# Kernel tuning notes

Hardware: AMD Instinct MI355X
Metric: run time of the kernel (lower is better)

The kernel has to match this reference:

```python
import jax, jax.numpy as jnp
import numpy as np
import itertools

G = 24  # octahedral rotation group order (reflection=False)
K = 3   # kernel_size

def _octahedral_tables():
    # 24 proper rotations of the cube as signed permutation matrices (det=+1)
    mats = []
    for perm in itertools.permutations(range(3)):
        for signs in itertoolsools_product if False else itertools.product((1, -1), repeat=3):
            M = np.zeros((3, 3), dtype=np.int64)
            for i, p in enumerate(perm):
                M[i, p] = signs[i]
            if round(np.linalg.det(M)) == 1:
                mats.append(M)
    mats = np.stack(mats)  # (24,3,3)
    key = {tuple(m.flatten()): i for i, m in enumerate(mats)}
    # Cayley-derived index shift: shift[g][h] = index of R_g^{-1} R_h
    shift = np.zeros((G, G), dtype=np.int64)
    for g in range(G):
        Rg_inv = mats[g].T  # orthogonal
        for h in range(G):
            shift[g, h] = key[tuple((Rg_inv @ mats[h]).flatten())]
    # spatial rotation gather indices: rotated K'(x) = K(R^{-1}(x-c)+c)
    c = (K - 1) // 2
    coords = np.stack(np.meshgrid(np.arange(K), np.arange(K), np.arange(K), indexing='ij'), -1).reshape(-1, 3)
    rot_idx = np.zeros((G, K ** 3), dtype=np.int64)
    for g in range(G):
        src = (coords - c) @ mats[g]  # equals R_g^{-1} @ (x-c) row-wise
        src = src + c
        rot_idx[g] = src[:, 0] * K * K + src[:, 1] * K + src[:, 2]
    return shift, rot_idx

SHIFT, ROT_IDX = _octahedral_tables()

def setup_inputs() -> dict:
    key = jax.random.key(0)
    k1, k2, k3, k4, k5 = jax.random.split(key, 5)
    B, I, O, H = 2, 16, 16, 32
    fan_g = I  # kaiming-ish scale for g_weight last dim
    fan_t = K ** 3
    return {
        'x': jax.random.normal(k1, (B, I, G, H, H, H), dtype=jnp.float32),
        'g_weight': jax.random.normal(k2, (G, O, I), dtype=jnp.float32) * (1.0 / np.sqrt(fan_g)),
        't_weight': jax.random.normal(k3, (O, 1, K, K, K), dtype=jnp.float32) * (1.0 / np.sqrt(fan_t)),
        'g_bias': jax.random.normal(k4, (1, O, 1, 1, 1, 1), dtype=jnp.float32) * 0.1,
        't_bias': jax.random.normal(k5, (1,), dtype=jnp.float32) * 0.1,
    }

def reference(x, g_weight, t_weight, g_bias, t_bias):
    O = g_weight.shape[1]
    B, _, _, H, W, D = x.shape
    # filter bank G: permute group axis of g_weight per group element -> (G_z, G_g, O, I)
    gfb = g_weight[SHIFT]
    # filter bank T: rotated depthwise kernels -> (O, G, K^3)
    tfb = t_weight.reshape(O, K ** 3)[:, ROT_IDX]
    w = tfb.reshape(O * G, 1, K, K, K)
    # group-equivariant channel mix + bias
    y = jnp.einsum('bighwd,zgoi->bozhwd', x, gfb) + g_bias
    y = y.reshape(B, O * G, H, W, D)
    # depthwise conv3d with groups = O*G, padding=1, stride=1
    out = jax.lax.conv_general_dilated(
        y, w, window_strides=(1, 1, 1), padding=[(1, 1)] * 3,
        dimension_numbers=('NCDHW', 'OIDHW', 'NCDHW'),
        feature_group_count=O * G) + t_bias[0]
    out = out.reshape(B, O, G, out.shape[2], out.shape[3], out.shape[4])
    return jax.nn.leaky_relu(out, negative_slope=0.01)
```

## Files before the change

### kernel.cpp

```cpp
#include <hip/hip_runtime.h>
#include <hip/hip_bf16.h>
#include <stdint.h>

typedef unsigned short ushortx;
typedef __attribute__((ext_vector_type(8))) short bs8;
typedef __attribute__((ext_vector_type(4))) float f32x4;

struct Tab {
    int shift[24][24];
    int rot[24][27];
};

constexpr Tab make_tab() {
    Tab t{};
    int mats[24][3][3] = {};
    {
        const int perms[6][3] = {{0,1,2},{0,2,1},{1,0,2},{1,2,0},{2,0,1},{2,1,0}};
        const int sgns[8][3]  = {{1,1,1},{1,1,-1},{1,-1,1},{1,-1,-1},
                                 {-1,1,1},{-1,1,-1},{-1,-1,1},{-1,-1,-1}};
        int n = 0;
        for (int pi = 0; pi < 6; ++pi)
            for (int si = 0; si < 8; ++si) {
                int M[3][3] = {};
                for (int i = 0; i < 3; ++i) M[i][perms[pi][i]] = sgns[si][i];
                int det = M[0][0]*(M[1][1]*M[2][2]-M[1][2]*M[2][1])
                        - M[0][1]*(M[1][0]*M[2][2]-M[1][2]*M[2][0])
                        + M[0][2]*(M[1][0]*M[2][1]-M[1][1]*M[2][0]);
                if (det == 1) {
                    for (int i = 0; i < 3; ++i)
                        for (int j = 0; j < 3; ++j) mats[n][i][j] = M[i][j];
                    ++n;
                }
            }
    }
    for (int g = 0; g < 24; ++g)
        for (int h = 0; h < 24; ++h) {
            int P[3][3] = {};
            for (int i = 0; i < 3; ++i)
                for (int j = 0; j < 3; ++j) {
                    int s = 0;
                    for (int e = 0; e < 3; ++e) s += mats[g][e][i] * mats[h][e][j];
                    P[i][j] = s;
                }
            for (int k = 0; k < 24; ++k) {
                bool eq = true;
                for (int i = 0; i < 3; ++i)
                    for (int j = 0; j < 3; ++j)
                        if (mats[k][i][j] != P[i][j]) eq = false;
                if (eq) t.shift[g][h] = k;
            }
        }
    for (int g = 0; g < 24; ++g)
        for (int j = 0; j < 27; ++j) {
            int co[3] = { j/9 - 1, (j/3)%3 - 1, j%3 - 1 };
            int src[3] = {};
            for (int d = 0; d < 3; ++d) {
                int s = 0;
                for (int e = 0; e < 3; ++e) s += co[e] * mats[g][e][d];
                src[d] = s + 1;
            }
            t.rot[g][j] = src[0]*9 + src[1]*3 + src[2];
        }
    return t;
}

__constant__ Tab TAB = make_tab();

#define GG 24
#define OO 16
#define II 16
#define PVOL 32768
#define MCH 384
#define KCH 384
#define KG  48

__device__ __forceinline__ unsigned f2bfu(float f) {
    union { float f; unsigned u; } a; a.f = f;
    unsigned r = a.u + 0x7FFFu + ((a.u >> 16) & 1u);
    return r >> 16;
}
__device__ __forceinline__ float bfu2f(unsigned h) {
    union { unsigned u; float f; } a; a.u = h << 16;
    return a.f;
}

#define GLOAD16(gp, lp) \
    __builtin_amdgcn_global_load_lds((const __attribute__((address_space(1))) void*)(gp), \
                                     (__attribute__((address_space(3))) void*)(lp), 16, 0, 0)

__global__ void build_weights2(const float* __restrict__ gw, const float* __restrict__ tw,
                               ushortx* __restrict__ w2, float* __restrict__ wt) {
    int idx = blockIdx.x * 256 + threadIdx.x;
    if (idx < MCH * KCH) {
        int m = idx / KCH, k = idx % KCH;
        int o = m / GG, z = m % GG;
        int i = k / GG, g = k % GG;
        float w = gw[TAB.shift[z][g] * (OO * II) + o * II + i];
        unsigned h = f2bfu(w);
        unsigned l = f2bfu(w - bfu2f(h));
        size_t base = (size_t)m * 768 + (k >> 5) * 64 + (k & 31);
        w2[base]      = (ushortx)h;
        w2[base + 32] = (ushortx)l;
    } else {
        int r = idx - MCH * KCH;
        if (r < MCH * 27) {
            int c = r / 27, j = r % 27;
            wt[r] = tw[(c / GG) * 27 + TAB.rot[c % GG][j]];
        }
    }
}

__global__ __launch_bounds__(256) void convert_x(const float* __restrict__ X,
                                                 uint4* __restrict__ Xhi,
                                                 uint4* __restrict__ Xlo) {
    const int n0 = blockIdx.x * 256, kg = blockIdx.y, b = blockIdx.z;
    __shared__ float s[8][260];
    const int t = threadIdx.x;
    const float* Xb = X + ((size_t)b * KCH + kg * 8) * PVOL;

    {
        const int r0 = t >> 6, c4 = (t & 63) * 4;
        float4 v0 = *(const float4*)&Xb[(size_t)r0 * PVOL + n0 + c4];
        float4 v1 = *(const float4*)&Xb[(size_t)(r0 + 4) * PVOL + n0 + c4];
        *(float4*)&s[r0][c4] = v0;
        *(float4*)&s[r0 + 4][c4] = v1;
    }
    __syncthreads();

    const int n = t;
    float f0 = s[0][n], f1 = s[1][n], f2 = s[2][n], f3 = s[3][n];
    float f4 = s[4][n], f5 = s[5][n], f6 = s[6][n], f7 = s[7][n];

    unsigned h0 = f2bfu(f0), h1 = f2bfu(f1), h2 = f2bfu(f2), h3 = f2bfu(f3);
    unsigned h4 = f2bfu(f4), h5 = f2bfu(f5), h6 = f2bfu(f6), h7 = f2bfu(f7);
    uint4 H = { h0 | (h1 << 16), h2 | (h3 << 16), h4 | (h5 << 16), h6 | (h7 << 16) };

    unsigned l0 = f2bfu(f0 - bfu2f(h0)), l1 = f2bfu(f1 - bfu2f(h1));
    unsigned l2 = f2bfu(f2 - bfu2f(h2)), l3 = f2bfu(f3 - bfu2f(h3));
    unsigned l4 = f2bfu(f4 - bfu2f(h4)), l5 = f2bfu(f5 - bfu2f(h5));
    unsigned l6 = f2bfu(f6 - bfu2f(h6)), l7 = f2bfu(f7 - bfu2f(h7));
    uint4 L = { l0 | (l1 << 16), l2 | (l3 << 16), l4 | (l5 << 16), l6 | (l7 << 16) };

    const size_t ci = ((size_t)(b * KG + kg)) * PVOL + n0 + n;
    Xhi[ci] = H;
    Xlo[ci] = L;
}

__global__ __launch_bounds__(256) void gemm_mfma(const ushortx* __restrict__ W2,
                                                 const uint4* __restrict__ Xhi,
                                                 const uint4* __restrict__ Xlo,
                                                 const float* __restrict__ gbias,
                                                 float* __restrict__ Y) {
    __shared__ ushortx As[2][8192];
    __shared__ ushortx Bs[2][8192];
    const int b = blockIdx.z, m0 = blockIdx.y * 128, n0 = blockIdx.x * 128;
    const int tid = threadIdx.x, lane = tid & 63, wave = tid >> 6;
    const int wr = wave >> 1, wc = wave & 1;
    const int l15 = lane & 15, lq = lane >> 4;

    f32x4 acc[4][4] = {};

    const char* Ab = (const char*)W2 + (size_t)m0 * 1536;
    const uint4* XH = Xhi + (size_t)b * KG * PVOL + n0;
    const uint4* XL = Xlo + (size_t)b * KG * PVOL + n0;

#define STAGE(bb, it)                                                          \
    {                                                                          \
        _Pragma("unroll")                                                      \
        for (int j = 0; j < 4; ++j) {                                          \
            int inst = j * 4 + wave;                                           \
            int fb = inst * 1024 + (lane << 4);                                \
            int row = fb >> 7;                                                 \
            int sch = ((fb >> 4) & 7) ^ (row & 7);                             \
            GLOAD16(Ab + (size_t)row * 1536 + (it) * 128 + sch * 16,           \
                    (char*)&As[bb][0] + fb);                                   \
            const uint4* plane = (sch < 4) ? XH : XL;                          \
            GLOAD16(plane + ((size_t)((it) * 4 + (sch & 3))) * PVOL + row,     \
                    (char*)&Bs[bb][0] + fb);                                   \
        }                                                                      \
    }

    STAGE(0, 0);

    int cur = 0;
    for (int it = 0; it < 12; ++it) {
        if (it < 11) {
            STAGE(cur ^ 1, it + 1);
            asm volatile("s_waitcnt vmcnt(8)" ::: "memory");
        } else {
            asm volatile("s_waitcnt vmcnt(0)" ::: "memory");
        }
        __builtin_amdgcn_sched_barrier(0);
        __builtin_amdgcn_s_barrier();
        __builtin_amdgcn_sched_barrier(0);

        bs8 ah[4], al[4], bh[4], bl[4];
        #pragma unroll
        for (int f = 0; f < 4; ++f) {
            int rowA = wr * 64 + f * 16 + l15;
            int swzA = (rowA & 7) << 4;
            ah[f] = *(const bs8*)((const char*)&As[cur][0] + rowA * 128 + ((lq * 16) ^ swzA));
            al[f] = *(const bs8*)((const char*)&As[cur][0] + rowA * 128 + ((64 + lq * 16) ^ swzA));
            int rowB = wc * 64 + f * 16 + l15;
            int swzB = (rowB & 7) << 4;
            bh[f] = *(const bs8*)((const char*)&Bs[cur][0] + rowB * 128 + ((lq * 16) ^ swzB));
            bl[f] = *(const bs8*)((const char*)&Bs[cur][0] + rowB * 128 + ((64 + lq * 16) ^ swzB));
        }
        #pragma unroll
        for (int fm = 0; fm < 4; ++fm)
            #pragma unroll
            for (int fn = 0; fn < 4; ++fn) {
                acc[fm][fn] = __builtin_amdgcn_mfma_f32_16x16x32_bf16(ah[fm], bh[fn], acc[fm][fn], 0, 0, 0);
                acc[fm][fn] = __builtin_amdgcn_mfma_f32_16x16x32_bf16(ah[fm], bl[fn], acc[fm][fn], 0, 0, 0);
                acc[fm][fn] = __builtin_amdgcn_mfma_f32_16x16x32_bf16(al[fm], bh[fn], acc[fm][fn], 0, 0, 0);
            }

        asm volatile("" ::: "memory");
        __builtin_amdgcn_s_barrier();
        asm volatile("" ::: "memory");
        cur ^= 1;
    }
#undef STAGE

    float* Yp = Y + (size_t)b * MCH * PVOL;
    #pragma unroll
    for (int fm = 0; fm < 4; ++fm)
        #pragma unroll
        for (int j = 0; j < 4; ++j) {
            int m = m0 + wr * 64 + fm * 16 + lq * 4 + j;
            float bias = gbias[m / GG];
            #pragma unroll
            for (int fn = 0; fn < 4; ++fn) {
                int n = n0 + wc * 64 + fn * 16 + l15;
                Yp[(size_t)m * PVOL + n] = acc[fm][fn][j] + bias;
            }
        }
}

__global__ __launch_bounds__(256) void dwconv(const float* __restrict__ Y,
                                              const float* __restrict__ Wt,
                                              const float* __restrict__ tb,
                                              float* __restrict__ O) {
    const int x0 = blockIdx.x * 4;
    const int c  = blockIdx.y;
    const int b  = blockIdx.z;
    const float* __restrict__ Yc = Y + ((size_t)(b * MCH + c)) * PVOL;
    float* __restrict__ Oc = O + ((size_t)(b * MCH + c)) * PVOL;

    __shared__ float s[6][34][40];
    __shared__ float taps[27];
    const int t = threadIdx.x;

    {
        float4 z4 = {0.f, 0.f, 0.f, 0.f};
        float4* sp = (float4*)s;
        for (int i = t; i < 2040; i += 256) sp[i] = z4;
    }
    if (t < 27) taps[t] = Wt[c * 27 + t];
    __syncthreads();

    const int y  = t >> 3;
    const int z0 = (t & 7) * 4;

    {
        float4 r[6];
        #pragma unroll
        for (int lx = 0; lx < 6; ++lx) {
            int x = x0 - 1 + lx;
            bool ok = (x >= 0 && x < 32);
            r[lx] = ok ? *(const float4*)&Yc[(size_t)x * 1024 + y * 32 + z0]
                       : (float4){0.f, 0.f, 0.f, 0.f};
        }
        #pragma unroll
        for (int lx = 0; lx < 6; ++lx)
            *(float4*)&s[lx][1 + y][4 + z0] = r[lx];
    }
    __syncthreads();

    const float t0 = tb[0];
    float w[27];
    #pragma unroll
    for (int j = 0; j < 27; ++j) w[j] = taps[j];

    float Wn[3][3][6];

    #define LOADWIN(slot, plane)                                              \
        {                                                                     \
            _Pragma("unroll")                                                 \
            for (int dy = 0; dy < 3; ++dy) {                                  \
                float4 a = *(const float4*)&s[plane][y + dy][z0];             \
                float4 bq = *(const float4*)&s[plane][y + dy][z0 + 4];        \
                float4 cq = *(const float4*)&s[plane][y + dy][z0 + 8];        \
                Wn[slot][dy][0] = a.w;                                        \
                Wn[slot][dy][1] = bq.x; Wn[slot][dy][2] = bq.y;               \
                Wn[slot][dy][3] = bq.z; Wn[slot][dy][4] = bq.w;               \
                Wn[slot][dy][5] = cq.x;                                       \
            }                                                                 \
        }

    LOADWIN(0, 0)
    LOADWIN(1, 1)

    #pragma unroll
    for (int xi = 0; xi < 4; ++xi) {
        LOADWIN((xi + 2) % 3, (xi + 2))
        const int s0 = xi % 3, s1 = (xi + 1) % 3, s2 = (xi + 2) % 3;
        float4 o;
        #pragma unroll
        for (int zz = 0; zz < 4; ++zz) {
            float a0 = 0.f, a1 = 0.f, a2 = 0.f;
            #pragma unroll
            for (int dy = 0; dy < 3; ++dy)
                #pragma unroll
                for (int dc = 0; dc < 3; ++dc) {
                    a0 += Wn[s0][dy][zz + dc] * w[dy * 3 + dc];
                    a1 += Wn[s1][dy][zz + dc] * w[9 + dy * 3 + dc];
                    a2 += Wn[s2][dy][zz + dc] * w[18 + dy * 3 + dc];
                }
            float v = a0 + a1 + a2 + t0;
            o[zz] = (v > 0.f) ? v : 0.01f * v;
        }
        *(float4*)&Oc[(size_t)(x0 + xi) * 1024 + y * 32 + z0] = o;
    }
    #undef LOADWIN
}

__global__ void build_weights(const float* __restrict__ gw, const float* __restrict__ tw,
                              float* __restrict__ wmix, float* __restrict__ wt) {
    int idx = blockIdx.x * 256 + threadIdx.x;
    if (idx < MCH * KCH) {
        int c = idx / KCH, k = idx % KCH;
        int o = c / GG, z = c % GG;
        int i = k / GG, g = k % GG;
        wmix[idx] = gw[TAB.shift[z][g] * (OO * II) + o * II + i];
    } else {
        int r = idx - MCH * KCH;
        if (r < MCH * 27) {
            int c = r / 27, j = r % 27;
            wt[r] = tw[(c / GG) * 27 + TAB.rot[c % GG][j]];
        }
    }
}

#define BM 128
#define BN 128
#define BK 16

__global__ __launch_bounds__(256) void gemm_mix(const float* __restrict__ A,
                                                const float* __restrict__ X,
                                                const float* __restrict__ gbias,
                                                float* __restrict__ Y) {
    const int b  = blockIdx.z;
    const int m0 = blockIdx.y * BM;
    const int n0 = blockIdx.x * BN;
    const float* __restrict__ Bp = X + (size_t)b * KCH * PVOL;
    float* __restrict__ Yp = Y + (size_t)b * MCH * PVOL;

    __shared__ float Ash[BK][BM];
    __shared__ float Bsh[BK][BN];

    const int tid = threadIdx.x;
    const int tx = tid % 16;
    const int ty = tid / 16;

    float acc[8][8] = {};

    for (int k0 = 0; k0 < KCH; k0 += BK) {
        #pragma unroll
        for (int r = 0; r < 2; ++r) {
            int tt = tid + r * 256;
            int m = tt / 4;
            int kk = (tt % 4) * 4;
            float4 v = *(const float4*)&A[(m0 + m) * KCH + k0 + kk];
            Ash[kk + 0][m] = v.x; Ash[kk + 1][m] = v.y;
            Ash[kk + 2][m] = v.z; Ash[kk + 3][m] = v.w;
        }
        #pragma unroll
        for (int r = 0; r < 2; ++r) {
            int tt = tid + r * 256;
            int kk = tt / 32;
            int n = (tt % 32) * 4;
            *(float4*)&Bsh[kk][n] = *(const float4*)&Bp[(size_t)(k0 + kk) * PVOL + n0 + n];
        }
        __syncthreads();
        #pragma unroll
        for (int kk = 0; kk < BK; ++kk) {
            float af[8], bf[8];
            #pragma unroll
            for (int i = 0; i < 4; ++i) {
                af[i]     = Ash[kk][ty * 4 + i];
                af[4 + i] = Ash[kk][64 + ty * 4 + i];
                bf[i]     = Bsh[kk][tx * 4 + i];
                bf[4 + i] = Bsh[kk][64 + tx * 4 + i];
            }
            #pragma unroll
            for (int i = 0; i < 8; ++i)
                #pragma unroll
                for (int j = 0; j < 8; ++j)
                    acc[i][j] += af[i] * bf[j];
        }
        __syncthreads();
    }

    #pragma unroll
    for (int i = 0; i < 8; ++i) {
        int m = m0 + ((i < 4) ? (ty * 4 + i) : (64 + ty * 4 + (i - 4)));
        float bias = gbias[m / GG];
        float4 v0 = { acc[i][0] + bias, acc[i][1] + bias, acc[i][2] + bias, acc[i][3] + bias };
        float4 v1 = { acc[i][4] + bias, acc[i][5] + bias, acc[i][6] + bias, acc[i][7] + bias };
        *(float4*)&Yp[(size_t)m * PVOL + n0 + tx * 4]      = v0;
        *(float4*)&Yp[(size_t)m * PVOL + n0 + 64 + tx * 4] = v1;
    }
}

extern "C" void kernel_launch(void* const* d_in, const int* in_sizes, int n_in,
                              void* d_out, int out_size, void* d_ws, size_t ws_size,
                              hipStream_t stream) {
    const float* x  = (const float*)d_in[0];
    const float* gw = (const float*)d_in[1];
    const float* tw = (const float*)d_in[2];
    const float* gb = (const float*)d_in[3];
    const float* tb = (const float*)d_in[4];
    float* out = (float*)d_out;
    float* ws  = (float*)d_ws;

    float*   wt   = ws;
    ushortx* w2   = (ushortx*)(ws + 10368);
    float*   wmix = ws + 10368;
    float*   y    = ws + 157824;
    uint4*   xhi  = (uint4*)(ws + 25323648);
    uint4*   xlo  = (uint4*)(ws + 37906560);

    const size_t need = (size_t)50489472 * 4;

    if (ws_size >= need) {
        build_weights2<<<dim3(617), dim3(256), 0, stream>>>(gw, tw, w2, wt);
        convert_x<<<dim3(128, KG, 2), dim3(256), 0, stream>>>(x, xhi, xlo);
        gemm_mfma<<<dim3(256, 3, 2), dim3(256), 0, stream>>>(w2, xhi, xlo, gb, y);
    } else {
        build_weights<<<dim3(617), dim3(256), 0, stream>>>(gw, tw, wmix, wt);
        gemm_mix<<<dim3(PVOL / BN, MCH / BM, 2), dim3(256), 0, stream>>>(wmix, x, gb, y);
    }
    dwconv<<<dim3(8, MCH, 2), dim3(256), 0, stream>>>(y, wt, tb, out);
}
```

Baseline: 305.2 us.

## Store GEMM intermediate as bf16 and stream depthwise conv over full x

The MFMA GEMM now writes its intermediate activation as bf16 instead of fp32, halving the write and re-read traffic for the large y tensor. The depthwise conv is restructured so that one block covers a whole channel volume and streams x-planes through a 4-slot ring buffer with register prefetch, which removes the 6-plane halo reloads. The GEMM's A tile becomes single-buffered so it can be loaded per iteration. The bf16 rounding of y adds extra precision loss, and the conv grid drops to MCH*2 blocks, each running a long serial loop.

```diff
diff --git a/kernel.cpp b/kernel.cpp
--- a/kernel.cpp
+++ b/kernel.cpp
@@ -150,8 +150,8 @@
                                                  const uint4* __restrict__ Xhi,
                                                  const uint4* __restrict__ Xlo,
                                                  const float* __restrict__ gbias,
-                                                 float* __restrict__ Y) {
-    __shared__ ushortx As[2][8192];
+                                                 ushortx* __restrict__ Y) {
+    __shared__ ushortx As[8192];
     __shared__ ushortx Bs[2][8192];
     const int b = blockIdx.z, m0 = blockIdx.y * 128, n0 = blockIdx.x * 128;
     const int tid = threadIdx.x, lane = tid & 63, wave = tid >> 6;
@@ -164,7 +164,7 @@
     const uint4* XH = Xhi + (size_t)b * KG * PVOL + n0;
     const uint4* XL = Xlo + (size_t)b * KG * PVOL + n0;
 
-#define STAGE(bb, it)                                                          \
+#define STAGE_A(it)                                                            \
     {                                                                          \
         _Pragma("unroll")                                                      \
         for (int j = 0; j < 4; ++j) {                                          \
@@ -173,20 +173,31 @@
             int row = fb >> 7;                                                 \
             int sch = ((fb >> 4) & 7) ^ (row & 7);                             \
             GLOAD16(Ab + (size_t)row * 1536 + (it) * 128 + sch * 16,           \
-                    (char*)&As[bb][0] + fb);                                   \
+                    (char*)As + fb);                                           \
+        }                                                                      \
+    }
+#define STAGE_B(bb, it)                                                        \
+    {                                                                          \
+        _Pragma("unroll")                                                      \
+        for (int j = 0; j < 4; ++j) {                                          \
+            int inst = j * 4 + wave;                                           \
+            int fb = inst * 1024 + (lane << 4);                                \
+            int row = fb >> 7;                                                 \
+            int sch = ((fb >> 4) & 7) ^ (row & 7);                             \
             const uint4* plane = (sch < 4) ? XH : XL;                          \
             GLOAD16(plane + ((size_t)((it) * 4 + (sch & 3))) * PVOL + row,     \
                     (char*)&Bs[bb][0] + fb);                                   \
         }                                                                      \
     }
 
-    STAGE(0, 0);
+    STAGE_B(0, 0);
 
     int cur = 0;
     for (int it = 0; it < 12; ++it) {
+        STAGE_A(it);
         if (it < 11) {
-            STAGE(cur ^ 1, it + 1);
-            asm volatile("s_waitcnt vmcnt(8)" ::: "memory");
+            STAGE_B(cur ^ 1, it + 1);
+            asm volatile("s_waitcnt vmcnt(4)" ::: "memory");
         } else {
             asm volatile("s_waitcnt vmcnt(0)" ::: "memory");
         }
@@ -199,8 +210,8 @@
         for (int f = 0; f < 4; ++f) {
             int rowA = wr * 64 + f * 16 + l15;
             int swzA = (rowA & 7) << 4;
-            ah[f] = *(const bs8*)((const char*)&As[cur][0] + rowA * 128 + ((lq * 16) ^ swzA));
-            al[f] = *(const bs8*)((const char*)&As[cur][0] + rowA * 128 + ((64 + lq * 16) ^ swzA));
+            ah[f] = *(const bs8*)((const char*)As + rowA * 128 + ((lq * 16) ^ swzA));
+            al[f] = *(const bs8*)((const char*)As + rowA * 128 + ((64 + lq * 16) ^ swzA));
             int rowB = wc * 64 + f * 16 + l15;
             int swzB = (rowB & 7) << 4;
             bh[f] = *(const bs8*)((const char*)&Bs[cur][0] + rowB * 128 + ((lq * 16) ^ swzB));
@@ -220,9 +231,10 @@
         asm volatile("" ::: "memory");
         cur ^= 1;
     }
-#undef STAGE
-
-    float* Yp = Y + (size_t)b * MCH * PVOL;
+#undef STAGE_A
+#undef STAGE_B
+
+    ushortx* Yp = Y + (size_t)b * MCH * PVOL;
     #pragma unroll
     for (int fm = 0; fm < 4; ++fm)
         #pragma unroll
@@ -232,50 +244,49 @@
             #pragma unroll
             for (int fn = 0; fn < 4; ++fn) {
                 int n = n0 + wc * 64 + fn * 16 + l15;
-                Yp[(size_t)m * PVOL + n] = acc[fm][fn][j] + bias;
+                Yp[(size_t)m * PVOL + n] = (ushortx)f2bfu(acc[fm][fn][j] + bias);
             }
         }
 }
 
-__global__ __launch_bounds__(256) void dwconv(const float* __restrict__ Y,
+__global__ __launch_bounds__(256) void dwconv(const ushortx* __restrict__ Y,
                                               const float* __restrict__ Wt,
                                               const float* __restrict__ tb,
                                               float* __restrict__ O) {
-    const int x0 = blockIdx.x * 4;
-    const int c  = blockIdx.y;
-    const int b  = blockIdx.z;
-    const float* __restrict__ Yc = Y + ((size_t)(b * MCH + c)) * PVOL;
+    const int c = blockIdx.x;
+    const int b = blockIdx.y;
+    const ushortx* __restrict__ Yc = Y + ((size_t)(b * MCH + c)) * PVOL;
     float* __restrict__ Oc = O + ((size_t)(b * MCH + c)) * PVOL;
 
-    __shared__ float s[6][34][40];
+    __shared__ float s[4][34][40];
     __shared__ float taps[27];
     const int t = threadIdx.x;
+    const int y  = t >> 3;
+    const int z0 = (t & 7) * 4;
+    const int yz = y * 32 + z0;
 
     {
         float4 z4 = {0.f, 0.f, 0.f, 0.f};
         float4* sp = (float4*)s;
-        for (int i = t; i < 2040; i += 256) sp[i] = z4;
+        for (int i = t; i < 4 * 34 * 40 / 4; i += 256) sp[i] = z4;
     }
     if (t < 27) taps[t] = Wt[c * 27 + t];
     __syncthreads();
 
-    const int y  = t >> 3;
-    const int z0 = (t & 7) * 4;
+#define LDP(a) ({                                                             \
+        ushort4 v_ = *(const ushort4*)&Yc[(size_t)(a) * 1024 + yz];           \
+        float4 f_;                                                            \
+        f_.x = bfu2f(v_.x); f_.y = bfu2f(v_.y);                               \
+        f_.z = bfu2f(v_.z); f_.w = bfu2f(v_.w);                               \
+        f_; })
 
     {
-        float4 r[6];
-        #pragma unroll
-        for (int lx = 0; lx < 6; ++lx) {
-            int x = x0 - 1 + lx;
-            bool ok = (x >= 0 && x < 32);
-            r[lx] = ok ? *(const float4*)&Yc[(size_t)x * 1024 + y * 32 + z0]
-                       : (float4){0.f, 0.f, 0.f, 0.f};
-        }
-        #pragma unroll
-        for (int lx = 0; lx < 6; ++lx)
-            *(float4*)&s[lx][1 + y][4 + z0] = r[lx];
+        float4 p0 = LDP(0), p1 = LDP(1);
+        *(float4*)&s[0][1 + y][4 + z0] = p0;
+        *(float4*)&s[1][1 + y][4 + z0] = p1;
     }
     __syncthreads();
+    float4 rplane = LDP(2);
 
     const float t0 = tb[0];
     float w[27];
@@ -284,45 +295,59 @@
 
     float Wn[3][3][6];
 
-    #define LOADWIN(slot, plane)                                              \
-        {                                                                     \
+#define LOADWIN(WS, LSLOT)                                                    \
+    {                                                                         \
+        _Pragma("unroll")                                                     \
+        for (int dy = 0; dy < 3; ++dy) {                                      \
+            float4 a_ = *(const float4*)&s[LSLOT][y + dy][z0];                \
+            float4 b_ = *(const float4*)&s[LSLOT][y + dy][z0 + 4];            \
+            float4 c_ = *(const float4*)&s[LSLOT][y + dy][z0 + 8];            \
+            Wn[WS][dy][0] = a_.w;                                             \
+            Wn[WS][dy][1] = b_.x; Wn[WS][dy][2] = b_.y;                       \
+            Wn[WS][dy][3] = b_.z; Wn[WS][dy][4] = b_.w;                       \
+            Wn[WS][dy][5] = c_.x;                                             \
+        }                                                                     \
+    }
+
+    LOADWIN(2, 3)
+    LOADWIN(0, 0)
+
+#define BODY(x, SA, SB, SC)                                                   \
+    {                                                                         \
+        float4 rn = ((x) + 3 < 32) ? LDP((x) + 3) : (float4){0.f,0.f,0.f,0.f};\
+        LOADWIN(SC, ((x) + 1) & 3)                                            \
+        float4 o;                                                             \
+        _Pragma("unroll")                                                     \
+        for (int zz = 0; zz < 4; ++zz) {                                      \
+            float a0 = 0.f, a1 = 0.f, a2 = 0.f;                               \
             _Pragma("unroll")                                                 \
-            for (int dy = 0; dy < 3; ++dy) {                                  \
-                float4 a = *(const float4*)&s[plane][y + dy][z0];             \
-                float4 bq = *(const float4*)&s[plane][y + dy][z0 + 4];        \
-                float4 cq = *(const float4*)&s[plane][y + dy][z0 + 8];        \
-                Wn[slot][dy][0] = a.w;                                        \
-                Wn[slot][dy][1] = bq.x; Wn[slot][dy][2] = bq.y;               \
-                Wn[slot][dy][3] = bq.z; Wn[slot][dy][4] = bq.w;               \
-                Wn[slot][dy][5] = cq.x;                                       \
-            }                                                                 \
-        }
-
-    LOADWIN(0, 0)
-    LOADWIN(1, 1)
-
-    #pragma unroll
-    for (int xi = 0; xi < 4; ++xi) {
-        LOADWIN((xi + 2) % 3, (xi + 2))
-        const int s0 = xi % 3, s1 = (xi + 1) % 3, s2 = (xi + 2) % 3;
-        float4 o;
-        #pragma unroll
-        for (int zz = 0; zz < 4; ++zz) {
-            float a0 = 0.f, a1 = 0.f, a2 = 0.f;
-            #pragma unroll
-            for (int dy = 0; dy < 3; ++dy)
-                #pragma unroll
-                for (int dc = 0; dc < 3; ++dc) {
-                    a0 += Wn[s0][dy][zz + dc] * w[dy * 3 + dc];
-                    a1 += Wn[s1][dy][zz + dc] * w[9 + dy * 3 + dc];
-                    a2 += Wn[s2][dy][zz + dc] * w[18 + dy * 3 + dc];
-                }
-            float v = a0 + a1 + a2 + t0;
-            o[zz] = (v > 0.f) ? v : 0.01f * v;
-        }
-        *(float4*)&Oc[(size_t)(x0 + xi) * 1024 + y * 32 + z0] = o;
-    }
-    #undef LOADWIN
+            for (int dy = 0; dy < 3; ++dy)                                    \
+                _Pragma("unroll")                                             \
+                for (int dc = 0; dc < 3; ++dc) {                              \
+                    a0 += Wn[SA][dy][zz + dc] * w[dy * 3 + dc];               \
+                    a1 += Wn[SB][dy][zz + dc] * w[9 + dy * 3 + dc];           \
+                    a2 += Wn[SC][dy][zz + dc] * w[18 + dy * 3 + dc];          \
+                }                                                             \
+            float v_ = a0 + a1 + a2 + t0;                                     \
+            o[zz] = (v_ > 0.f) ? v_ : 0.01f * v_;                             \
+        }                                                                     \
+        *(float4*)&Oc[(size_t)(x) * 1024 + yz] = o;                           \
+        *(float4*)&s[((x) + 2) & 3][1 + y][4 + z0] = rplane;                  \
+        asm volatile("s_waitcnt lgkmcnt(0)" ::: "memory");                    \
+        __builtin_amdgcn_s_barrier();                                         \
+        rplane = rn;                                                          \
+    }
+
+    for (int xb = 0; xb < 30; xb += 3) {
+        BODY(xb + 0, 2, 0, 1)
+        BODY(xb + 1, 0, 1, 2)
+        BODY(xb + 2, 1, 2, 0)
+    }
+    BODY(30, 2, 0, 1)
+    BODY(31, 0, 1, 2)
+#undef BODY
+#undef LOADWIN
+#undef LDP
 }
 
 __global__ void build_weights(const float* __restrict__ gw, const float* __restrict__ tw,
@@ -342,22 +367,18 @@
     }
 }
 
-#define BM 128
-#define BN 128
-#define BK 16
-
 __global__ __launch_bounds__(256) void gemm_mix(const float* __restrict__ A,
                                                 const float* __restrict__ X,
                                                 const float* __restrict__ gbias,
-                                                float* __restrict__ Y) {
+                                                float* __restrict__ Yp_) {
     const int b  = blockIdx.z;
-    const int m0 = blockIdx.y * BM;
-    const int n0 = blockIdx.x * BN;
+    const int m0 = blockIdx.y * 128;
+    const int n0 = blockIdx.x * 128;
     const float* __restrict__ Bp = X + (size_t)b * KCH * PVOL;
-    float* __restrict__ Yp = Y + (size_t)b * MCH * PVOL;
-
-    __shared__ float Ash[BK][BM];
-    __shared__ float Bsh[BK][BN];
+    float* __restrict__ Yp = Yp_ + (size_t)b * MCH * PVOL;
+
+    __shared__ float Ash[16][128];
+    __shared__ float Bsh[16][128];
 
     const int tid = threadIdx.x;
     const int tx = tid % 16;
@@ -365,7 +386,7 @@
 
     float acc[8][8] = {};
 
-    for (int k0 = 0; k0 < KCH; k0 += BK) {
+    for (int k0 = 0; k0 < KCH; k0 += 16) {
         #pragma unroll
         for (int r = 0; r < 2; ++r) {
             int tt = tid + r * 256;
@@ -384,7 +405,7 @@
         }
         __syncthreads();
         #pragma unroll
-        for (int kk = 0; kk < BK; ++kk) {
+        for (int kk = 0; kk < 16; ++kk) {
             float af[8], bf[8];
             #pragma unroll
             for (int i = 0; i < 4; ++i) {
@@ -413,6 +434,94 @@
     }
 }
 
+__global__ __launch_bounds__(256) void dwconv_f32(const float* __restrict__ Y,
+                                                  const float* __restrict__ Wt,
+                                                  const float* __restrict__ tb,
+                                                  float* __restrict__ O) {
+    const int x0 = blockIdx.x * 4;
+    const int c  = blockIdx.y;
+    const int b  = blockIdx.z;
+    const float* __restrict__ Yc = Y + ((size_t)(b * MCH + c)) * PVOL;
+    float* __restrict__ Oc = O + ((size_t)(b * MCH + c)) * PVOL;
+
+    __shared__ float s[6][34][40];
+    __shared__ float taps[27];
+    const int t = threadIdx.x;
+
+    {
+        float4 z4 = {0.f, 0.f, 0.f, 0.f};
+        float4* sp = (float4*)s;
+        for (int i = t; i < 2040; i += 256) sp[i] = z4;
+    }
+    if (t < 27) taps[t] = Wt[c * 27 + t];
+    __syncthreads();
+
+    const int y  = t >> 3;
+    const int z0 = (t & 7) * 4;
+
+    {
+        float4 r[6];
+        #pragma unroll
+        for (int lx = 0; lx < 6; ++lx) {
+            int x = x0 - 1 + lx;
+            bool ok = (x >= 0 && x < 32);
+            r[lx] = ok ? *(const float4*)&Yc[(size_t)x * 1024 + y * 32 + z0]
+                       : (float4){0.f, 0.f, 0.f, 0.f};
+        }
+        #pragma unroll
+        for (int lx = 0; lx < 6; ++lx)
+            *(float4*)&s[lx][1 + y][4 + z0] = r[lx];
+    }
+    __syncthreads();
+
+    const float t0 = tb[0];
+    float w[27];
+    #pragma unroll
+    for (int j = 0; j < 27; ++j) w[j] = taps[j];
+
+    float Wn[3][3][6];
+
+    #define LOADWIN(slot, plane)                                              \
+        {                                                                     \
+            _Pragma("unroll")                                                 \
+            for (int dy = 0; dy < 3; ++dy) {                                  \
+                float4 a = *(const float4*)&s[plane][y + dy][z0];             \
+                float4 bq = *(const float4*)&s[plane][y + dy][z0 + 4];        \
+                float4 cq = *(const float4*)&s[plane][y + dy][z0 + 8];        \
+                Wn[slot][dy][0] = a.w;                                        \
+                Wn[slot][dy][1] = bq.x; Wn[slot][dy][2] = bq.y;               \
+                Wn[slot][dy][3] = bq.z; Wn[slot][dy][4] = bq.w;               \
+                Wn[slot][dy][5] = cq.x;                                       \
+            }                                                                 \
+        }
+
+    LOADWIN(0, 0)
+    LOADWIN(1, 1)
+
+    #pragma unroll
+    for (int xi = 0; xi < 4; ++xi) {
+        LOADWIN((xi + 2) % 3, (xi + 2))
+        const int s0 = xi % 3, s1 = (xi + 1) % 3, s2 = (xi + 2) % 3;
+        float4 o;
+        #pragma unroll
+        for (int zz = 0; zz < 4; ++zz) {
+            float a0 = 0.f, a1 = 0.f, a2 = 0.f;
+            #pragma unroll
+            for (int dy = 0; dy < 3; ++dy)
+                #pragma unroll
+                for (int dc = 0; dc < 3; ++dc) {
+                    a0 += Wn[s0][dy][zz + dc] * w[dy * 3 + dc];
+                    a1 += Wn[s1][dy][zz + dc] * w[9 + dy * 3 + dc];
+                    a2 += Wn[s2][dy][zz + dc] * w[18 + dy * 3 + dc];
+                }
+            float v = a0 + a1 + a2 + t0;
+            o[zz] = (v > 0.f) ? v : 0.01f * v;
+        }
+        *(float4*)&Oc[(size_t)(x0 + xi) * 1024 + y * 32 + z0] = o;
+    }
+    #undef LOADWIN
+}
+
 extern "C" void kernel_launch(void* const* d_in, const int* in_sizes, int n_in,
                               void* d_out, int out_size, void* d_ws, size_t ws_size,
                               hipStream_t stream) {
@@ -424,22 +533,24 @@
     float* out = (float*)d_out;
     float* ws  = (float*)d_ws;
 
-    float*   wt   = ws;
-    ushortx* w2   = (ushortx*)(ws + 10368);
-    float*   wmix = ws + 10368;
-    float*   y    = ws + 157824;
-    uint4*   xhi  = (uint4*)(ws + 25323648);
-    uint4*   xlo  = (uint4*)(ws + 37906560);
+    float*   wt    = ws;
+    ushortx* w2    = (ushortx*)(ws + 10368);
+    float*   wmix  = ws + 10368;
+    ushortx* y16   = (ushortx*)(ws + 157824);
+    float*   y32   = ws + 157824;
+    uint4*   xhi   = (uint4*)(ws + 25323648);
+    uint4*   xlo   = (uint4*)(ws + 37906560);
 
     const size_t need = (size_t)50489472 * 4;
 
     if (ws_size >= need) {
         build_weights2<<<dim3(617), dim3(256), 0, stream>>>(gw, tw, w2, wt);
         convert_x<<<dim3(128, KG, 2), dim3(256), 0, stream>>>(x, xhi, xlo);
-        gemm_mfma<<<dim3(256, 3, 2), dim3(256), 0, stream>>>(w2, xhi, xlo, gb, y);
+        gemm_mfma<<<dim3(256, 3, 2), dim3(256), 0, stream>>>(w2, xhi, xlo, gb, y16);
+        dwconv<<<dim3(MCH, 2), dim3(256), 0, stream>>>(y16, wt, tb, out);
     } else {
         build_weights<<<dim3(617), dim3(256), 0, stream>>>(gw, tw, wmix, wt);
-        gemm_mix<<<dim3(PVOL / BN, MCH / BM, 2), dim3(256), 0, stream>>>(wmix, x, gb, y);
-    }
-    dwconv<<<dim3(8, MCH, 2), dim3(256), 0, stream>>>(y, wt, tb, out);
-}
+        gemm_mix<<<dim3(PVOL / 128, MCH / 128, 2), dim3(256), 0, stream>>>(wmix, x, gb, y32);
+        dwconv_f32<<<dim3(8, MCH, 2), dim3(256), 0, stream>>>(y32, wt, tb, out);
+    }
+}
```

After: 298.2 us. 2.3% less time.
